# Kernel optimization log

Hardware: AMD Instinct MI355X
Metric: run time of the kernel (lower is better)

## Reference

```python
import jax, jax.numpy as jnp
import numpy as np

N = 50000      # nodes
E = 800000     # edges
ZD = 64        # intrinsic latent dim (ambient = ZD+1)
H = 256        # hidden_dim
RADIUS = 1.0
EPS = 1e-7


def _lin_init(k, fi, fo):
    s = 1.0 / np.sqrt(fi)
    kw, kb = jax.random.split(k)
    return (jax.random.uniform(kw, (fi, fo), minval=-s, maxval=s),
            jax.random.uniform(kb, (fo,), minval=-s, maxval=s))


def setup_inputs() -> dict:
    key = jax.random.key(0)
    ks = jax.random.split(key, 12)
    # sample z on the hyperboloid: exp map at mu0 of a tangent vector (0, u)
    u = jax.random.normal(ks[0], (N, ZD), dtype=jnp.float32) * 0.5
    nrm = jnp.linalg.norm(u, axis=-1, keepdims=True)
    z = jnp.concatenate([RADIUS * jnp.cosh(nrm / RADIUS),
                         RADIUS * jnp.sinh(nrm / RADIUS) * u / jnp.maximum(nrm, 1e-8)],
                        axis=-1)  # [N, ZD+1]
    edge_index = jax.random.randint(ks[1], (2, E), 0, N, dtype=jnp.int64)
    W1, b1 = _lin_init(ks[2], ZD + 1, H)
    W2, b2 = _lin_init(ks[3], H, H)
    W3, b3 = _lin_init(ks[4], H, H)
    W4, b4 = _lin_init(ks[5], H, H // 2)
    rW1, rb1 = _lin_init(ks[6], H, H)
    rW2, rb2 = _lin_init(ks[7], H, 1)
    tW1, tb1 = _lin_init(ks[8], H, H)
    tW2, tb2 = _lin_init(ks[9], H, 1)
    return {"z": z, "edge_index": edge_index,
            "W1": W1, "b1": b1, "W2": W2, "b2": b2,
            "W3": W3, "b3": b3, "W4": W4, "b4": b4,
            "rW1": rW1, "rb1": rb1, "rW2": rW2, "rb2": rb2,
            "tW1": tW1, "tb1": tb1, "tW2": tW2, "tb2": tb2}


def _lorentz_inner(x, y):
    return -x[..., 0] * y[..., 0] + jnp.sum(x[..., 1:] * y[..., 1:], axis=-1)


def hyperboloid_dist(x, y, R):
    alpha = jnp.clip(-_lorentz_inner(x, y) / (R * R), 1.0 + EPS, None)
    return R * jnp.arccosh(alpha)


def inverse_exp_map_mu0(x, R):
    # log map at mu0 = (R,0,...,0); result has zero time component
    alpha = jnp.clip(x[..., 0:1] / R, 1.0 + EPS, None)
    d = R * jnp.arccosh(alpha)
    coef = d / (R * jnp.sqrt(alpha * alpha - 1.0))
    return jnp.concatenate([jnp.zeros_like(x[..., :1]), coef * x[..., 1:]], axis=-1)


def gcn_conv(x, W, b, src, dst, n):
    # PyG GCNConv: add self loops, symmetric normalization
    h = x @ W  # [N, Fout]
    deg = jnp.zeros((n,), h.dtype).at[dst].add(1.0) + 1.0
    dinv = deg ** -0.5
    norm = dinv[src] * dinv[dst]  # [E]
    out = jax.ops.segment_sum(h[src] * norm[:, None], dst, num_segments=n)
    out = out + h / deg[:, None]  # self-loop term (deg^-1)
    return out + b


def reference(z, edge_index, W1, b1, W2, b2, W3, b3, W4, b4,
              rW1, rb1, rW2, rb2, tW1, tb1, tW2, tb2):
    src, dst = edge_index[0], edge_index[1]
    z_mu0 = inverse_exp_map_mu0(z, RADIUS)
    dist = -hyperboloid_dist(z[src], z[dst], RADIUS)  # [E]
    # GNN stack (r and t branches share the SAME layers in the source)
    h = gcn_conv(z_mu0, W1, b1, src, dst, N)
    h = gcn_conv(jax.nn.relu(h), W2, b2, src, dst, N)
    h = gcn_conv(jax.nn.relu(h), W3, b3, src, dst, N)
    h = gcn_conv(jax.nn.relu(h), W4, b4, src, dst, N)  # [N, H/2]
    inp = jnp.concatenate([h[src], h[dst]], axis=1)  # [E, H]
    r = (jax.nn.leaky_relu(inp @ rW1 + rb1, 0.2) @ rW2 + rb2)[:, 0]
    t = (jax.nn.leaky_relu(inp @ tW1 + tb1, 0.2) @ tW2 + tb2)[:, 0]
    return jax.nn.sigmoid((dist - r) / t)
```

## Files before the change

kernel.cpp:

```cpp
#include <hip/hip_runtime.h>
#include <hip/hip_bf16.h>
#include <math.h>

typedef __hip_bfloat16 bf16;

#define N_NODES 50000
#define N_EDGES 800000
#define DIM 65

__device__ __forceinline__ float b2f(bf16 x) { return __bfloat162float(x); }
__device__ __forceinline__ bf16 f2b(float x) { return __float2bfloat16(x); }

__device__ __forceinline__ double zread(const void* z, int f32m, size_t i) {
    return f32m ? (double)((const float*)z)[i] : (double)b2f(((const bf16*)z)[i]);
}
__device__ __forceinline__ float zreadf(const void* z, int f32m, size_t i) {
    return f32m ? ((const float*)z)[i] : b2f(((const bf16*)z)[i]);
}

__global__ void probe_kernel(const void* z, const void* ei, int* flags) {
    __shared__ int bad_f32;
    __shared__ int nonzero_hi;
    int t = threadIdx.x;
    if (t == 0) { bad_f32 = 0; nonzero_hi = 0; }
    __syncthreads();
    {
        int node = t * 97;
        float v = ((const float*)z)[node * DIM];
        if (!(v >= 1.0f && v <= 1.0e6f)) atomicAdd(&bad_f32, 1);
    }
    {
        int k = t * 3121;
        if (((const int*)ei)[2 * k + 1] != 0) atomicAdd(&nonzero_hi, 1);
    }
    __syncthreads();
    if (t == 0) {
        flags[0] = (bad_f32 < 8) ? 1 : 0;
        flags[1] = (nonzero_hi < 128) ? 1 : 0;
    }
}

__global__ void norm_d_kernel(const void* __restrict__ in, const int* __restrict__ flags,
                              double* __restrict__ out, int n) {
    int i = blockIdx.x * 256 + threadIdx.x;
    if (i < n)
        out[i] = flags[0] ? (double)((const float*)in)[i]
                          : (double)b2f(((const bf16*)in)[i]);
}

__global__ void norm_e_kernel(const void* __restrict__ ei, const int* __restrict__ flags,
                              int* __restrict__ srcb, int* __restrict__ dstb) {
    int e = blockIdx.x * 256 + threadIdx.x;
    if (e >= N_EDGES) return;
    const int* p = (const int*)ei;
    if (flags[1]) {
        srcb[e] = p[2 * e];
        dstb[e] = p[2 * N_EDGES + 2 * e];
    } else {
        srcb[e] = p[e];
        dstb[e] = p[N_EDGES + e];
    }
}

__global__ void coef_kernel(const void* __restrict__ z, const int* __restrict__ flags,
                            double* __restrict__ coefd) {
    int n = blockIdx.x * 256 + threadIdx.x;
    if (n >= N_NODES) return;
    int f32m = flags[0];
    double a = fmax(zread(z, f32m, (size_t)n * DIM), 1.0 + 1e-7);
    coefd[n] = acosh(a) / sqrt(a * a - 1.0);
}

__global__ void hist_kernel(const int* __restrict__ dst, int* __restrict__ cnt) {
    int e = blockIdx.x * 256 + threadIdx.x;
    if (e < N_EDGES) atomicAdd(&cnt[dst[e]], 1);
}

__global__ void deg_kernel(const int* __restrict__ cnt, double* __restrict__ degf,
                           double* __restrict__ dinv) {
    int n = blockIdx.x * 256 + threadIdx.x;
    if (n < N_NODES) {
        double dg = (double)cnt[n] + 1.0;
        degf[n] = dg;
        dinv[n] = 1.0 / sqrt(dg);
    }
}

__global__ void scan_kernel(const int* __restrict__ cnt, int* __restrict__ rowptr) {
    __shared__ int sh[1024];
    __shared__ int carry;
    int tid = threadIdx.x;
    if (tid == 0) { carry = 0; rowptr[0] = 0; }
    __syncthreads();
    for (int base = 0; base < N_NODES; base += 1024) {
        int i = base + tid;
        int v = (i < N_NODES) ? cnt[i] : 0;
        sh[tid] = v;
        __syncthreads();
        for (int off = 1; off < 1024; off <<= 1) {
            int add = (tid >= off) ? sh[tid - off] : 0;
            __syncthreads();
            sh[tid] += add;
            __syncthreads();
        }
        if (i < N_NODES) rowptr[i + 1] = carry + sh[tid];
        int total = sh[1023];
        __syncthreads();
        if (tid == 0) carry += total;
        __syncthreads();
    }
}

__global__ void fill_kernel(const int* __restrict__ src, const int* __restrict__ dst,
                            const int* __restrict__ rowptr, int* __restrict__ fillc,
                            const double* __restrict__ dinv,
                            int* __restrict__ csr_src, float* __restrict__ csr_norm) {
    int e = blockIdx.x * 256 + threadIdx.x;
    if (e >= N_EDGES) return;
    int s = src[e], d = dst[e];
    int pos = atomicAdd(&fillc[d], 1);
    int idx = rowptr[d] + pos;
    csr_src[idx] = s;
    csr_norm[idx] = (float)(dinv[s] * dinv[d]);
}

__global__ void dist_zone_kernel(const void* __restrict__ zf, const int* __restrict__ flags,
                                 const int* __restrict__ src, const int* __restrict__ dst,
                                 double* __restrict__ dist) {
    int e = blockIdx.x * 4 + (threadIdx.x >> 6);
    int lane = threadIdx.x & 63;
    int f32m = flags[0];
    int s = src[e], d = dst[e];
    size_t sb = (size_t)s * DIM, db = (size_t)d * DIM;
    float p = __fmul_rn(zreadf(zf, f32m, sb + 1 + lane),
                        zreadf(zf, f32m, db + 1 + lane));
    p = __fadd_rn(p, __shfl_xor(p, 32));
    p = __fadd_rn(p, __shfl_xor(p, 16));
    p = __fadd_rn(p, __shfl_xor(p, 8));
    p = __fadd_rn(p, __shfl_xor(p, 4));
    p = __fadd_rn(p, __shfl_xor(p, 2));
    p = __fadd_rn(p, __shfl_xor(p, 1));
    if (lane == 0) {
        float m = __fmul_rn(zreadf(zf, f32m, sb), zreadf(zf, f32m, db));
        float alpha = __fsub_rn(m, p);
        const float clip32 = 1.00000011920928955e+00f;
        const double clip = 1.00000011920928955078125;
        double u = ldexp(1.0, ilogb((double)fmaxf(m, 2.0f)) - 23);
        double dd;
        if (alpha <= clip32) {
            dd = -acosh(clip + 0.08 * u);
        } else if ((double)alpha - clip <= 1.5 * u) {
            dd = -acosh(clip + 0.25 * u);
        } else {
            dd = -(double)acoshf(alpha);
        }
        dist[e] = dd;
    }
}

template <int MODE>
__global__ __launch_bounds__(256) void gemm64_kernel(
    const float* __restrict__ X, int ldx,
    const double* __restrict__ W, int ldw,
    float* __restrict__ out, int ldo,
    int M, int K,
    const void* __restrict__ zraw, const int* __restrict__ flags,
    const double* __restrict__ coefd) {
    __shared__ float  As[16][68];
    __shared__ double Bs[16][66];
    const int t = threadIdx.x;
    const int tx = t & 15, ty = t >> 4;
    const int r0 = blockIdx.x * 64, c0 = blockIdx.y * 64;
    const int rl = t >> 2, j0 = (t & 3) * 4;
    const int r = r0 + rl;
    const int f32m = (MODE == 2) ? flags[0] : 0;
    const double cf = (MODE == 2 && r < M) ? coefd[r] : 0.0;
    double acc[4][4] = {{0.0}};
    for (int kc = 0; kc < K; kc += 16) {
        #pragma unroll
        for (int jj = 0; jj < 4; ++jj) {
            int k = kc + j0 + jj;
            float v = 0.f;
            if (r < M && k < K) {
                if (MODE == 2) {
                    v = (k == 0) ? 0.f : (float)(cf * zread(zraw, f32m, (size_t)r * DIM + k));
                } else {
                    v = X[(size_t)r * ldx + k];
                    if (MODE == 1) v = fmaxf(v, 0.f);
                }
            }
            As[j0 + jj][rl] = v;
        }
        {
            const int jb = t >> 6, cb = t & 63;
            #pragma unroll
            for (int jj = 0; jj < 4; ++jj) {
                int j = jj * 4 + jb;
                int k = kc + j;
                Bs[j][cb] = (k < K) ? W[(size_t)k * ldw + c0 + cb] : 0.0;
            }
        }
        __syncthreads();
        #pragma unroll
        for (int j = 0; j < 16; ++j) {
            double a[4], b[4];
            #pragma unroll
            for (int i = 0; i < 4; ++i) a[i] = (double)As[j][ty * 4 + i];
            #pragma unroll
            for (int q = 0; q < 4; ++q) b[q] = Bs[j][tx * 4 + q];
            #pragma unroll
            for (int i = 0; i < 4; ++i)
                #pragma unroll
                for (int q = 0; q < 4; ++q)
                    acc[i][q] += a[i] * b[q];
        }
        __syncthreads();
    }
    #pragma unroll
    for (int i = 0; i < 4; ++i) {
        int rr = r0 + ty * 4 + i;
        if (rr < M) {
            float4 v = make_float4((float)acc[i][0], (float)acc[i][1],
                                   (float)acc[i][2], (float)acc[i][3]);
            *(float4*)&out[(size_t)rr * ldo + c0 + tx * 4] = v;
        }
    }
}

__global__ void agg_kernel(const float* __restrict__ hpre, const int* __restrict__ rowptr,
                           const int* __restrict__ csr_src, const float* __restrict__ csr_norm,
                           const double* __restrict__ degf, const double* __restrict__ b,
                           float* __restrict__ out, int F) {
    int n = blockIdx.x;
    int f = threadIdx.x;
    int beg = rowptr[n], end = rowptr[n + 1];
    double acc = (double)hpre[(size_t)n * F + f] / degf[n];
    for (int i = beg; i < end; ++i) {
        acc += (double)csr_norm[i] * (double)hpre[(size_t)csr_src[i] * F + f];
    }
    out[(size_t)n * F + f] = (float)(acc + b[f]);
}

template <int FIRST>
__global__ __launch_bounds__(256) void edge_reduce_kernel(
    const float* __restrict__ P, const float* __restrict__ Q,
    const int* __restrict__ src, const int* __restrict__ dst,
    const double* __restrict__ b1c, const double* __restrict__ W2c,
    const double* __restrict__ b2, double* __restrict__ outv) {
    __shared__ double b1s[128];
    __shared__ double w2s[128];
    int t = threadIdx.x;
    if (t < 128) { b1s[t] = b1c[t]; w2s[t] = W2c[t]; }
    __syncthreads();
    int e = blockIdx.x * 4 + (t >> 6);
    int lane = t & 63;
    int s = src[e], d = dst[e];
    float2 p2 = *(const float2*)&P[(size_t)s * 128 + lane * 2];
    float2 q2 = *(const float2*)&Q[(size_t)d * 128 + lane * 2];
    double h0 = (double)p2.x + (double)q2.x + b1s[2 * lane];
    double h1 = (double)p2.y + (double)q2.y + b1s[2 * lane + 1];
    h0 = (h0 > 0.0) ? h0 : 0.2 * h0;
    h1 = (h1 > 0.0) ? h1 : 0.2 * h1;
    double acc = h0 * w2s[2 * lane] + h1 * w2s[2 * lane + 1];
    #pragma unroll
    for (int off = 1; off < 64; off <<= 1) acc += __shfl_xor(acc, off);
    if (lane == 0) {
        if (FIRST) outv[e] = acc + b2[0];
        else       outv[e] += acc;
    }
}

__global__ void combine_kernel(const double* __restrict__ dist, const double* __restrict__ rv,
                               const double* __restrict__ tv, const int* __restrict__ flags,
                               void* __restrict__ out) {
    int e = blockIdx.x * 256 + threadIdx.x;
    double x = (dist[e] - rv[e]) / tv[e];
    double sg = 1.0 / (1.0 + exp(-x));
    if (flags[0]) ((float*)out)[e] = (float)sg;
    else          ((bf16*)out)[e] = f2b((float)sg);
}

extern "C" void kernel_launch(void* const* d_in, const int* in_sizes, int n_in,
                              void* d_out, int out_size, void* d_ws, size_t ws_size,
                              hipStream_t stream) {
    (void)in_sizes; (void)n_in; (void)out_size; (void)ws_size;
    const void* z_raw  = d_in[0];
    const void* ei_raw = d_in[1];

    char* w = (char*)d_ws;
    auto alloc = [&](size_t bytes) {
        char* p = w;
        w += (bytes + 255) & ~(size_t)255;
        return p;
    };
    float*  hpre  = (float*)alloc((size_t)N_NODES * 256 * 4);
    float*  hagg  = (float*)alloc((size_t)N_NODES * 256 * 4);
    double* coefd = (double*)alloc((size_t)N_NODES * 8);
    double* dist  = (double*)alloc((size_t)N_EDGES * 8);
    double* rv    = (double*)alloc((size_t)N_EDGES * 8);
    double* tv    = (double*)alloc((size_t)N_EDGES * 8);
    int*    srcb  = (int*)alloc((size_t)N_EDGES * 4);
    int*    dstb  = (int*)alloc((size_t)N_EDGES * 4);
    int*    csr_s = (int*)alloc((size_t)N_EDGES * 4);
    float*  csr_n = (float*)alloc((size_t)N_EDGES * 4);
    int*    rowptr= (int*)alloc((size_t)(N_NODES + 1) * 4);
    int*    cnt   = (int*)alloc((size_t)N_NODES * 4);
    int*    fillc = (int*)alloc((size_t)N_NODES * 4);
    double* degf  = (double*)alloc((size_t)N_NODES * 8);
    double* dinv  = (double*)alloc((size_t)N_NODES * 8);
    int*    flags = (int*)alloc(256);
    double* W1d  = (double*)alloc((size_t)DIM * 256 * 8);
    double* W2d  = (double*)alloc((size_t)256 * 256 * 8);
    double* W3d  = (double*)alloc((size_t)256 * 256 * 8);
    double* W4d  = (double*)alloc((size_t)256 * 128 * 8);
    double* b1d  = (double*)alloc(256 * 8);
    double* b2d  = (double*)alloc(256 * 8);
    double* b3d  = (double*)alloc(256 * 8);
    double* b4d  = (double*)alloc(128 * 8);
    double* rW1d = (double*)alloc((size_t)256 * 256 * 8);
    double* rb1d = (double*)alloc(256 * 8);
    double* rW2d = (double*)alloc(256 * 8);
    double* rb2d = (double*)alloc(8);
    double* tW1d = (double*)alloc((size_t)256 * 256 * 8);
    double* tb1d = (double*)alloc(256 * 8);
    double* tW2d = (double*)alloc(256 * 8);
    double* tb2d = (double*)alloc(8);

    float* Ptab = hpre;
    float* Qtab = hpre + (size_t)N_NODES * 128;

    hipMemsetAsync(cnt, 0, (size_t)N_NODES * 4, stream);
    hipMemsetAsync(fillc, 0, (size_t)N_NODES * 4, stream);

    probe_kernel<<<1, 256, 0, stream>>>(z_raw, ei_raw, flags);

    auto normd = [&](const void* in, double* out, int n) {
        norm_d_kernel<<<(n + 255) / 256, 256, 0, stream>>>(in, flags, out, n);
    };
    normd(d_in[2],  W1d,  DIM * 256);  normd(d_in[3],  b1d,  256);
    normd(d_in[4],  W2d,  256 * 256);  normd(d_in[5],  b2d,  256);
    normd(d_in[6],  W3d,  256 * 256);  normd(d_in[7],  b3d,  256);
    normd(d_in[8],  W4d,  256 * 128);  normd(d_in[9],  b4d,  128);
    normd(d_in[10], rW1d, 256 * 256);  normd(d_in[11], rb1d, 256);
    normd(d_in[12], rW2d, 256);        normd(d_in[13], rb2d, 1);
    normd(d_in[14], tW1d, 256 * 256);  normd(d_in[15], tb1d, 256);
    normd(d_in[16], tW2d, 256);        normd(d_in[17], tb2d, 1);
    norm_e_kernel<<<(N_EDGES + 255) / 256, 256, 0, stream>>>(ei_raw, flags, srcb, dstb);

    coef_kernel<<<196, 256, 0, stream>>>(z_raw, flags, coefd);
    hist_kernel<<<3125, 256, 0, stream>>>(dstb, cnt);
    deg_kernel<<<196, 256, 0, stream>>>(cnt, degf, dinv);
    scan_kernel<<<1, 1024, 0, stream>>>(cnt, rowptr);
    fill_kernel<<<3125, 256, 0, stream>>>(srcb, dstb, rowptr, fillc, dinv, csr_s, csr_n);
    dist_zone_kernel<<<200000, 256, 0, stream>>>(z_raw, flags, srcb, dstb, dist);

    gemm64_kernel<2><<<dim3(782, 4), 256, 0, stream>>>(nullptr, DIM, W1d, 256, hpre, 256,
                                                       N_NODES, DIM, z_raw, flags, coefd);
    agg_kernel<<<N_NODES, 256, 0, stream>>>(hpre, rowptr, csr_s, csr_n, degf, b1d, hagg, 256);
    gemm64_kernel<1><<<dim3(782, 4), 256, 0, stream>>>(hagg, 256, W2d, 256, hpre, 256,
                                                       N_NODES, 256, nullptr, nullptr, nullptr);
    agg_kernel<<<N_NODES, 256, 0, stream>>>(hpre, rowptr, csr_s, csr_n, degf, b2d, hagg, 256);
    gemm64_kernel<1><<<dim3(782, 4), 256, 0, stream>>>(hagg, 256, W3d, 256, hpre, 256,
                                                       N_NODES, 256, nullptr, nullptr, nullptr);
    agg_kernel<<<N_NODES, 256, 0, stream>>>(hpre, rowptr, csr_s, csr_n, degf, b3d, hagg, 256);
    gemm64_kernel<1><<<dim3(782, 2), 256, 0, stream>>>(hagg, 256, W4d, 128, hpre, 128,
                                                       N_NODES, 256, nullptr, nullptr, nullptr);
    agg_kernel<<<N_NODES, 128, 0, stream>>>(hpre, rowptr, csr_s, csr_n, degf, b4d, hagg, 128);

    for (int br = 0; br < 2; ++br) {
        const double* bW1 = br ? tW1d : rW1d;
        const double* bb1 = br ? tb1d : rb1d;
        const double* bW2 = br ? tW2d : rW2d;
        const double* bb2 = br ? tb2d : rb2d;
        double* outv = br ? tv : rv;
        for (int c = 0; c < 2; ++c) {
            gemm64_kernel<0><<<dim3(782, 2), 256, 0, stream>>>(
                hagg, 128, bW1 + c * 128, 256, Ptab, 128,
                N_NODES, 128, nullptr, nullptr, nullptr);
            gemm64_kernel<0><<<dim3(782, 2), 256, 0, stream>>>(
                hagg, 128, bW1 + (size_t)128 * 256 + c * 128, 256, Qtab, 128,
                N_NODES, 128, nullptr, nullptr, nullptr);
            if (c == 0)
                edge_reduce_kernel<1><<<200000, 256, 0, stream>>>(
                    Ptab, Qtab, srcb, dstb, bb1 + c * 128, bW2 + c * 128, bb2, outv);
            else
                edge_reduce_kernel<0><<<200000, 256, 0, stream>>>(
                    Ptab, Qtab, srcb, dstb, bb1 + c * 128, bW2 + c * 128, bb2, outv);
        }
    }

    combine_kernel<<<3125, 256, 0, stream>>>(dist, rv, tv, flags, (void*)d_out);
}
```

Baseline: 2.868 ms.

## Enlarge GEMM row tile to 128, merge P/Q GEMMs, parallelize CSR scan

The fp64-accumulating GEMM now computes a 128x64 tile per block (8x4 outputs per thread), which halves the grid and reuses each loaded B tile across twice as many rows. The two per-chunk P and Q GEMMs in the edge MLP become one GEMM over a repacked 128x256 weight matrix, writing an interleaved PQ table that the edge reduction reads by offset. The single-block scan switches from a serial loop of 1024-wide Blelloch passes to per-thread chunk sums plus one block scan. Costs include higher register pressure from 32 double accumulators, which may lower occupancy, and an extra small repack launch per chunk.

```diff
diff --git a/kernel.cpp b/kernel.cpp
--- a/kernel.cpp
+++ b/kernel.cpp
@@ -87,28 +87,24 @@
 }
 
 __global__ void scan_kernel(const int* __restrict__ cnt, int* __restrict__ rowptr) {
-    __shared__ int sh[1024];
-    __shared__ int carry;
-    int tid = threadIdx.x;
-    if (tid == 0) { carry = 0; rowptr[0] = 0; }
+    __shared__ int tot[1024];
+    int t = threadIdx.x;
+    const int CH = (N_NODES + 1023) / 1024;
+    int beg = t * CH;
+    int end = beg + CH; if (end > N_NODES) end = N_NODES;
+    int s = 0;
+    for (int i = beg; i < end; ++i) s += cnt[i];
+    tot[t] = s;
     __syncthreads();
-    for (int base = 0; base < N_NODES; base += 1024) {
-        int i = base + tid;
-        int v = (i < N_NODES) ? cnt[i] : 0;
-        sh[tid] = v;
+    for (int off = 1; off < 1024; off <<= 1) {
+        int add = (t >= off) ? tot[t - off] : 0;
         __syncthreads();
-        for (int off = 1; off < 1024; off <<= 1) {
-            int add = (tid >= off) ? sh[tid - off] : 0;
-            __syncthreads();
-            sh[tid] += add;
-            __syncthreads();
-        }
-        if (i < N_NODES) rowptr[i + 1] = carry + sh[tid];
-        int total = sh[1023];
+        tot[t] += add;
         __syncthreads();
-        if (tid == 0) carry += total;
-        __syncthreads();
-    }
+    }
+    int run = (t == 0) ? 0 : tot[t - 1];
+    if (t == 0) rowptr[0] = 0;
+    for (int i = beg; i < end; ++i) { run += cnt[i]; rowptr[i + 1] = run; }
 }
 
 __global__ void fill_kernel(const int* __restrict__ src, const int* __restrict__ dst,
@@ -166,50 +162,55 @@
     int M, int K,
     const void* __restrict__ zraw, const int* __restrict__ flags,
     const double* __restrict__ coefd) {
-    __shared__ float  As[16][68];
+    __shared__ float  As[16][132];
     __shared__ double Bs[16][66];
     const int t = threadIdx.x;
-    const int tx = t & 15, ty = t >> 4;
-    const int r0 = blockIdx.x * 64, c0 = blockIdx.y * 64;
-    const int rl = t >> 2, j0 = (t & 3) * 4;
-    const int r = r0 + rl;
+    const int tx = t & 15;
+    const int ty = t >> 4;
+    const int r0 = blockIdx.x * 128, c0 = blockIdx.y * 64;
+    const int arl = t >> 1;
+    const int aj0 = (t & 1) * 8;
+    const int bj  = t >> 4;
+    const int bc0 = (t & 15) * 4;
+    const int ar = r0 + arl;
     const int f32m = (MODE == 2) ? flags[0] : 0;
-    const double cf = (MODE == 2 && r < M) ? coefd[r] : 0.0;
-    double acc[4][4] = {{0.0}};
+    const double cf = (MODE == 2 && ar < M) ? coefd[ar] : 0.0;
+    double acc[8][4];
+    #pragma unroll
+    for (int i = 0; i < 8; ++i)
+        #pragma unroll
+        for (int q = 0; q < 4; ++q) acc[i][q] = 0.0;
     for (int kc = 0; kc < K; kc += 16) {
         #pragma unroll
-        for (int jj = 0; jj < 4; ++jj) {
-            int k = kc + j0 + jj;
+        for (int jj = 0; jj < 8; ++jj) {
+            int k = kc + aj0 + jj;
             float v = 0.f;
-            if (r < M && k < K) {
+            if (ar < M && k < K) {
                 if (MODE == 2) {
-                    v = (k == 0) ? 0.f : (float)(cf * zread(zraw, f32m, (size_t)r * DIM + k));
+                    v = (k == 0) ? 0.f : (float)(cf * zread(zraw, f32m, (size_t)ar * DIM + k));
                 } else {
-                    v = X[(size_t)r * ldx + k];
+                    v = X[(size_t)ar * ldx + k];
                     if (MODE == 1) v = fmaxf(v, 0.f);
                 }
             }
-            As[j0 + jj][rl] = v;
+            As[aj0 + jj][arl] = v;
         }
         {
-            const int jb = t >> 6, cb = t & 63;
+            int k = kc + bj;
             #pragma unroll
-            for (int jj = 0; jj < 4; ++jj) {
-                int j = jj * 4 + jb;
-                int k = kc + j;
-                Bs[j][cb] = (k < K) ? W[(size_t)k * ldw + c0 + cb] : 0.0;
-            }
+            for (int q = 0; q < 4; ++q)
+                Bs[bj][bc0 + q] = (k < K) ? W[(size_t)k * ldw + c0 + bc0 + q] : 0.0;
         }
         __syncthreads();
         #pragma unroll
         for (int j = 0; j < 16; ++j) {
-            double a[4], b[4];
+            double a[8], b[4];
             #pragma unroll
-            for (int i = 0; i < 4; ++i) a[i] = (double)As[j][ty * 4 + i];
+            for (int i = 0; i < 8; ++i) a[i] = (double)As[j][ty * 8 + i];
             #pragma unroll
             for (int q = 0; q < 4; ++q) b[q] = Bs[j][tx * 4 + q];
             #pragma unroll
-            for (int i = 0; i < 4; ++i)
+            for (int i = 0; i < 8; ++i)
                 #pragma unroll
                 for (int q = 0; q < 4; ++q)
                     acc[i][q] += a[i] * b[q];
@@ -217,14 +218,24 @@
         __syncthreads();
     }
     #pragma unroll
-    for (int i = 0; i < 4; ++i) {
-        int rr = r0 + ty * 4 + i;
+    for (int i = 0; i < 8; ++i) {
+        int rr = r0 + ty * 8 + i;
         if (rr < M) {
             float4 v = make_float4((float)acc[i][0], (float)acc[i][1],
                                    (float)acc[i][2], (float)acc[i][3]);
             *(float4*)&out[(size_t)rr * ldo + c0 + tx * 4] = v;
         }
     }
+}
+
+__global__ void repack_kernel(const double* __restrict__ W1, int c,
+                              double* __restrict__ Bpq) {
+    int idx = blockIdx.x * 256 + threadIdx.x;
+    if (idx >= 128 * 256) return;
+    int k = idx >> 8, j = idx & 255;
+    double v = (j < 128) ? W1[(size_t)k * 256 + c * 128 + j]
+                         : W1[(size_t)(128 + k) * 256 + c * 128 + (j - 128)];
+    Bpq[idx] = v;
 }
 
 __global__ void agg_kernel(const float* __restrict__ hpre, const int* __restrict__ rowptr,
@@ -243,7 +254,7 @@
 
 template <int FIRST>
 __global__ __launch_bounds__(256) void edge_reduce_kernel(
-    const float* __restrict__ P, const float* __restrict__ Q,
+    const float* __restrict__ PQ,
     const int* __restrict__ src, const int* __restrict__ dst,
     const double* __restrict__ b1c, const double* __restrict__ W2c,
     const double* __restrict__ b2, double* __restrict__ outv) {
@@ -255,8 +266,8 @@
     int e = blockIdx.x * 4 + (t >> 6);
     int lane = t & 63;
     int s = src[e], d = dst[e];
-    float2 p2 = *(const float2*)&P[(size_t)s * 128 + lane * 2];
-    float2 q2 = *(const float2*)&Q[(size_t)d * 128 + lane * 2];
+    float2 p2 = *(const float2*)&PQ[(size_t)s * 256 + lane * 2];
+    float2 q2 = *(const float2*)&PQ[(size_t)d * 256 + 128 + lane * 2];
     double h0 = (double)p2.x + (double)q2.x + b1s[2 * lane];
     double h1 = (double)p2.y + (double)q2.y + b1s[2 * lane + 1];
     h0 = (h0 > 0.0) ? h0 : 0.2 * h0;
@@ -309,6 +320,7 @@
     double* degf  = (double*)alloc((size_t)N_NODES * 8);
     double* dinv  = (double*)alloc((size_t)N_NODES * 8);
     int*    flags = (int*)alloc(256);
+    double* Bpq   = (double*)alloc((size_t)128 * 256 * 8);
     double* W1d  = (double*)alloc((size_t)DIM * 256 * 8);
     double* W2d  = (double*)alloc((size_t)256 * 256 * 8);
     double* W3d  = (double*)alloc((size_t)256 * 256 * 8);
@@ -326,8 +338,7 @@
     double* tW2d = (double*)alloc(256 * 8);
     double* tb2d = (double*)alloc(8);
 
-    float* Ptab = hpre;
-    float* Qtab = hpre + (size_t)N_NODES * 128;
+    float* PQ = hpre;
 
     hipMemsetAsync(cnt, 0, (size_t)N_NODES * 4, stream);
     hipMemsetAsync(fillc, 0, (size_t)N_NODES * 4, stream);
@@ -354,16 +365,16 @@
     fill_kernel<<<3125, 256, 0, stream>>>(srcb, dstb, rowptr, fillc, dinv, csr_s, csr_n);
     dist_zone_kernel<<<200000, 256, 0, stream>>>(z_raw, flags, srcb, dstb, dist);
 
-    gemm64_kernel<2><<<dim3(782, 4), 256, 0, stream>>>(nullptr, DIM, W1d, 256, hpre, 256,
+    gemm64_kernel<2><<<dim3(391, 4), 256, 0, stream>>>(nullptr, DIM, W1d, 256, hpre, 256,
                                                        N_NODES, DIM, z_raw, flags, coefd);
     agg_kernel<<<N_NODES, 256, 0, stream>>>(hpre, rowptr, csr_s, csr_n, degf, b1d, hagg, 256);
-    gemm64_kernel<1><<<dim3(782, 4), 256, 0, stream>>>(hagg, 256, W2d, 256, hpre, 256,
+    gemm64_kernel<1><<<dim3(391, 4), 256, 0, stream>>>(hagg, 256, W2d, 256, hpre, 256,
                                                        N_NODES, 256, nullptr, nullptr, nullptr);
     agg_kernel<<<N_NODES, 256, 0, stream>>>(hpre, rowptr, csr_s, csr_n, degf, b2d, hagg, 256);
-    gemm64_kernel<1><<<dim3(782, 4), 256, 0, stream>>>(hagg, 256, W3d, 256, hpre, 256,
+    gemm64_kernel<1><<<dim3(391, 4), 256, 0, stream>>>(hagg, 256, W3d, 256, hpre, 256,
                                                        N_NODES, 256, nullptr, nullptr, nullptr);
     agg_kernel<<<N_NODES, 256, 0, stream>>>(hpre, rowptr, csr_s, csr_n, degf, b3d, hagg, 256);
-    gemm64_kernel<1><<<dim3(782, 2), 256, 0, stream>>>(hagg, 256, W4d, 128, hpre, 128,
+    gemm64_kernel<1><<<dim3(391, 2), 256, 0, stream>>>(hagg, 256, W4d, 128, hpre, 128,
                                                        N_NODES, 256, nullptr, nullptr, nullptr);
     agg_kernel<<<N_NODES, 128, 0, stream>>>(hpre, rowptr, csr_s, csr_n, degf, b4d, hagg, 128);
 
@@ -374,18 +385,16 @@
         const double* bb2 = br ? tb2d : rb2d;
         double* outv = br ? tv : rv;
         for (int c = 0; c < 2; ++c) {
-            gemm64_kernel<0><<<dim3(782, 2), 256, 0, stream>>>(
-                hagg, 128, bW1 + c * 128, 256, Ptab, 128,
-                N_NODES, 128, nullptr, nullptr, nullptr);
-            gemm64_kernel<0><<<dim3(782, 2), 256, 0, stream>>>(
-                hagg, 128, bW1 + (size_t)128 * 256 + c * 128, 256, Qtab, 128,
+            repack_kernel<<<128, 256, 0, stream>>>(bW1, c, Bpq);
+            gemm64_kernel<0><<<dim3(391, 4), 256, 0, stream>>>(
+                hagg, 128, Bpq, 256, PQ, 256,
                 N_NODES, 128, nullptr, nullptr, nullptr);
             if (c == 0)
                 edge_reduce_kernel<1><<<200000, 256, 0, stream>>>(
-                    Ptab, Qtab, srcb, dstb, bb1 + c * 128, bW2 + c * 128, bb2, outv);
+                    PQ, srcb, dstb, bb1 + c * 128, bW2 + c * 128, bb2, outv);
             else
                 edge_reduce_kernel<0><<<200000, 256, 0, stream>>>(
-                    Ptab, Qtab, srcb, dstb, bb1 + c * 128, bW2 + c * 128, bb2, outv);
+                    PQ, srcb, dstb, bb1 + c * 128, bW2 + c * 128, bb2, outv);
         }
     }
 
```

After: 2.895 ms. About the same (+0.9%).
